# Performance work log

Measured on AMD Instinct MI355X. Metric: run time of the kernel, lower is better.

The kernel has to match this reference:

```python
import jax, jax.numpy as jnp
import numpy as np

N, E, D_IN, H, OUT = 50000, 800000, 128, 256, 2
BN_EPS = 1e-5
LN_EPS = 1e-5


def _xavier(k, fi, fo):
    lim = float(np.sqrt(6.0 / (fi + fo)))
    return jax.random.uniform(k, (fi, fo), minval=-lim, maxval=lim, dtype=jnp.float32)


def setup_inputs() -> dict:
    key = jax.random.key(0)
    ks = jax.random.split(key, 8)
    return {
        "x": jax.random.normal(ks[0], (N, D_IN), dtype=jnp.float32),
        "edge_index": jax.random.randint(ks[1], (2, E), 0, N, dtype=jnp.int32),
        "feature_scale": jnp.ones((D_IN,), jnp.float32),
        "feature_bias": jnp.zeros((D_IN,), jnp.float32),
        "bn0_g": jnp.ones((D_IN,), jnp.float32),
        "bn0_b": jnp.zeros((D_IN,), jnp.float32),
        "W1": _xavier(ks[2], D_IN, H), "b1": jnp.zeros((H,), jnp.float32),
        "bn1_g": jnp.ones((H,), jnp.float32), "bn1_b": jnp.zeros((H,), jnp.float32),
        "ln1_g": jnp.ones((H,), jnp.float32), "ln1_b": jnp.zeros((H,), jnp.float32),
        "W2": _xavier(ks[3], H, H), "b2": jnp.zeros((H,), jnp.float32),
        "bn2_g": jnp.ones((H,), jnp.float32), "bn2_b": jnp.zeros((H,), jnp.float32),
        "ln2_g": jnp.ones((H,), jnp.float32), "ln2_b": jnp.zeros((H,), jnp.float32),
        "Wout": _xavier(ks[4], H, OUT), "bout": jnp.zeros((OUT,), jnp.float32),
    }


def _batchnorm(x, g, b):
    # training-mode BatchNorm1d: batch stats over node axis, biased variance
    mu = jnp.mean(x, axis=0)
    var = jnp.mean(jnp.square(x - mu), axis=0)
    return g * (x - mu) * jax.lax.rsqrt(var + BN_EPS) + b


def _layernorm(x, g, b):
    mu = jnp.mean(x, axis=-1, keepdims=True)
    var = jnp.mean(jnp.square(x - mu), axis=-1, keepdims=True)
    return g * (x - mu) * jax.lax.rsqrt(var + LN_EPS) + b


def _gcn(x, W, b, src, dst, dinv):
    # PyG GCNConv with self-loops: D^{-1/2}(A+I)D^{-1/2} X W + b
    h = x @ W                                   # [N, F]
    norm = (dinv[src] * dinv[dst])[:, None]     # [E, 1]
    msg = h[src] * norm                         # [E, F] (dominant traffic)
    agg = jax.ops.segment_sum(msg, dst, num_segments=N)
    return agg + (dinv * dinv)[:, None] * h + b


def _forward(x, feature_scale, feature_bias, bn0_g, bn0_b,
             W1, b1, bn1_g, bn1_b, ln1_g, ln1_b,
             W2, b2, bn2_g, bn2_b, ln2_g, ln2_b,
             Wout, bout, edge_index):
    src, dst = edge_index[0], edge_index[1]
    deg = jax.ops.segment_sum(jnp.ones((E,), x.dtype), dst, num_segments=N) + 1.0
    dinv = jax.lax.rsqrt(deg)

    h = x * feature_scale + feature_bias
    h = _batchnorm(h, bn0_g, bn0_b)            # input_bn; dropout = identity (eval)

    # layer 0 (no residual: i == 0)
    h1 = _gcn(h, W1, b1, src, dst, dinv)
    h1 = jax.nn.relu(h1)
    h1 = _batchnorm(h1, bn1_g, bn1_b)
    h1 = _layernorm(h1, ln1_g, ln1_b)

    # layer 1 (residual add, shapes match)
    h2 = _gcn(h1, W2, b2, src, dst, dinv)
    h2 = jax.nn.relu(h2)
    h2 = _batchnorm(h2, bn2_g, bn2_b)
    h2 = _layernorm(h2, ln2_g, ln2_b)
    h2 = h2 + h1

    return h2 @ Wout + bout


def reference(x, edge_index, feature_scale, feature_bias, bn0_g, bn0_b,
              W1, b1, bn1_g, bn1_b, ln1_g, ln1_b,
              W2, b2, bn2_g, bn2_b, ln2_g, ln2_b,
              Wout, bout):
    return _forward(x, feature_scale, feature_bias, bn0_g, bn0_b,
                    W1, b1, bn1_g, bn1_b, ln1_g, ln1_b,
                    W2, b2, bn2_g, bn2_b, ln2_g, ln2_b,
                    Wout, bout, edge_index)
```

## Files before the change

kernel.cpp:

```cpp
#include <hip/hip_runtime.h>
#include <hip/hip_bf16.h>
#include <stdint.h>

#define N_NODES 50000
#define N_EDGES 800000
#define D_IN    128
#define H_DIM   256
#define BN_EPS  1e-5f
#define LN_EPS  1e-5f
#define NBLK2 782
#define SLICE_ELEMS ((size_t)N_NODES * 32)
#define EDGE_CHUNK 4096
#define BN0_BLOCKS 1024
#define TR_BLOCKS 256
#define NBKT 196
#define CHUNK 2048
#define RCHUNKS 391

typedef float v4f __attribute__((ext_vector_type(4)));
typedef float v2f __attribute__((ext_vector_type(2)));
typedef short v8s __attribute__((ext_vector_type(8)));
typedef unsigned v4u __attribute__((ext_vector_type(4)));

__device__ __forceinline__ float bflo(unsigned u){ return __uint_as_float(u << 16); }
__device__ __forceinline__ float bfhi(unsigned u){ return __uint_as_float(u & 0xffff0000u); }
__device__ __forceinline__ unsigned short f2bf(float f){
  unsigned u = __float_as_uint(f);
  u += 0x7fffu + ((u >> 16) & 1u);
  return (unsigned short)(u >> 16);
}
__device__ __forceinline__ unsigned pack2(float a, float b){
  return (unsigned)f2bf(a) | ((unsigned)f2bf(b) << 16);
}

__device__ __forceinline__ int block_excl_scan(int v){
  int t = threadIdx.x;
  int lane = t & 63, w = t >> 6;
  int inc = v;
  #pragma unroll
  for (int m = 1; m < 64; m <<= 1){
    int o = __shfl_up(inc, m, 64);
    if (lane >= m) inc += o;
  }
  __shared__ int wsum[4];
  if (lane == 63) wsum[w] = inc;
  __syncthreads();
  int base = 0;
  #pragma unroll
  for (int j = 0; j < 4; ++j) if (j < w) base += wsum[j];
  return base + inc - v;
}

__global__ __launch_bounds__(256) void bn0r1_k(const int* ei, const float* x,
                                               const float* fs, const float* fb,
                                               float* S, float* Q, int* ghist){
  int b = blockIdx.x, t = threadIdx.x;
  if (b >= BN0_BLOCKS){
    __shared__ int lh[NBKT];
    int b2 = b - BN0_BLOCKS;
    for (int i = t; i < NBKT; i += 256) lh[i] = 0;
    __syncthreads();
    int e0 = b2 * CHUNK;
    int n = min(CHUNK, N_EDGES - e0);
    for (int i = t; i < n; i += 256)
      atomicAdd(&lh[ei[N_EDGES + e0 + i] >> 8], 1);
    __syncthreads();
    if (t < NBKT && lh[t] > 0) atomicAdd(&ghist[t], lh[t]);
    return;
  }
  int cl = t & 31, rg = t >> 5;
  int c = cl * 4;
  float4 fs4 = *(const float4*)(fs + c);
  float4 fb4 = *(const float4*)(fb + c);
  float s0=0,s1=0,s2=0,s3=0,q0=0,q1=0,q2=0,q3=0;
  for (int row = b * 8 + rg; row < N_NODES; row += BN0_BLOCKS * 8){
    float4 xv = *(const float4*)(x + (size_t)row * D_IN + c);
    float v0 = xv.x * fs4.x + fb4.x;
    float v1 = xv.y * fs4.y + fb4.y;
    float v2 = xv.z * fs4.z + fb4.z;
    float v3 = xv.w * fs4.w + fb4.w;
    s0 += v0; s1 += v1; s2 += v2; s3 += v3;
    q0 += v0*v0; q1 += v1*v1; q2 += v2*v2; q3 += v3*v3;
  }
  __shared__ float red[256][8];
  red[t][0]=s0; red[t][1]=s1; red[t][2]=s2; red[t][3]=s3;
  red[t][4]=q0; red[t][5]=q1; red[t][6]=q2; red[t][7]=q3;
  __syncthreads();
  float* Sr = S + (b & 7) * D_IN;
  float* Qr = Q + (b & 7) * D_IN;
  if (t < 32){
    float a[8];
    #pragma unroll
    for (int i = 0; i < 8; ++i) a[i] = red[t][i];
    for (int j = 1; j < 8; ++j)
      #pragma unroll
      for (int i = 0; i < 8; ++i) a[i] += red[t + 32*j][i];
    #pragma unroll
    for (int i = 0; i < 4; ++i){ atomicAdd(&Sr[t*4+i], a[i]); atomicAdd(&Qr[t*4+i], a[4+i]); }
  }
}

__global__ __launch_bounds__(256) void r3_k(const int* ei, const int* ghist, int* gcursor, unsigned* ebuf){
  __shared__ unsigned short dstS[CHUNK];
  __shared__ int lh[NBKT], cb[NBKT], sbb[NBKT];
  int t = threadIdx.x;
  int v = (t < NBKT) ? ghist[t] : 0;
  int epre = block_excl_scan(v);
  if (t < NBKT){ sbb[t] = epre; lh[t] = 0; }
  __syncthreads();
  int e0 = blockIdx.x * CHUNK;
  int n = min(CHUNK, N_EDGES - e0);
  for (int i = t; i < n; i += 256){
    int d = ei[N_EDGES + e0 + i];
    dstS[i] = (unsigned short)d;
    atomicAdd(&lh[d >> 8], 1);
  }
  __syncthreads();
  if (t < NBKT && lh[t] > 0) cb[t] = sbb[t] + atomicAdd(&gcursor[t], lh[t]);
  __syncthreads();
  if (t < NBKT) lh[t] = 0;
  __syncthreads();
  for (int i = t; i < n; i += 256){
    int d = dstS[i];
    int bkt = d >> 8;
    int r = atomicAdd(&lh[bkt], 1);
    unsigned src = (unsigned)ei[e0 + i];
    ebuf[cb[bkt] + r] = ((unsigned)(d & 255) << 16) | src;
  }
}

__global__ __launch_bounds__(256) void sortprep_k(const unsigned* ebuf, const int* ghist,
                                                  int* perm, int* offs, float* dinv,
                                                  unsigned short* edges,
                                                  const float* W1, const float* W2,
                                                  unsigned short* W1t, unsigned short* W2t){
  int b = blockIdx.x, t = threadIdx.x;
  if (b < NBKT){
    __shared__ int h[256], dh[128], ep_s[128], W_s[128], lc[128], curs[256], sbb[NBKT + 1];
    int gv = (t < NBKT) ? ghist[t] : 0;
    int gpre = block_excl_scan(gv);
    if (t < NBKT) sbb[t] = gpre;
    if (t == NBKT - 1) sbb[NBKT] = gpre + gv;
    h[t] = 0;
    if (t < 128){ dh[t] = 0; lc[t] = 0; }
    __syncthreads();
    int lo = sbb[b], hi = sbb[b + 1];
    for (int i = lo + t; i < hi; i += 256)
      atomicAdd(&h[(ebuf[i] >> 16) & 255], 1);
    __syncthreads();
    int node = b * 256 + t;
    bool valid = node < N_NODES;
    int deg = valid ? h[t] : 0;
    if (valid) atomicAdd(&dh[min(deg, 127)], 1);
    __syncthreads();
    int cv = (t < 128) ? dh[t] : 0;
    int e1 = block_excl_scan(cv);
    __syncthreads();
    int e2 = block_excl_scan((t < 128) ? cv * t : 0);
    __syncthreads();
    if (t < 128){ ep_s[t] = e1; W_s[t] = e2; }
    __syncthreads();
    if (valid){
      int bin = min(deg, 127);
      int r = atomicAdd(&lc[bin], 1);
      int pl = ep_s[bin] + r;
      int pos = b * 256 + pl;
      int off = lo + W_s[bin] + (pl - ep_s[bin]) * deg;
      perm[pos] = node;
      offs[pos] = off;
      dinv[node] = rsqrtf((float)deg + 1.0f);
      curs[t] = off;
    }
    __syncthreads();
    for (int i = lo + t; i < hi; i += 256){
      unsigned u = ebuf[i];
      int l8 = (u >> 16) & 255;
      int pos = atomicAdd(&curs[l8], 1);
      edges[pos] = (unsigned short)(u & 0xffffu);
    }
    if (b == 0 && t == 0) offs[N_NODES] = N_EDGES;
    return;
  }
  int i = (b - NBKT) * 256 + t;
  if (i < D_IN * H_DIM){
    int r = i / H_DIM, c = i % H_DIM;
    W1t[c * D_IN + r] = f2bf(W1[i]);
  }
  if (i < H_DIM * H_DIM){
    int r = i / H_DIM, c = i % H_DIM;
    W2t[c * H_DIM + r] = f2bf(W2[i]);
  }
}

__global__ __launch_bounds__(512) void gemm1_k(const float* x, const float* S, const float* Q,
                                               const float* fs, const float* fb,
                                               const float* gg, const float* bb,
                                               const unsigned short* Bt, const float* dinv,
                                               unsigned short* C, int M){
  __shared__ __align__(16) short smem[16896];
  __shared__ float ac[128], cc[128], dvs[128];
  short* As = smem;
  short* Bs = smem + 128 * 40;
  int t = threadIdx.x;
  int m0 = blockIdx.x * 128;
  int lane = t & 63, w = t >> 6;
  int wr = w >> 2, wc = w & 3;
  int fr = lane & 15, quad = lane >> 4;
  if (t < 128){
    dvs[t] = (m0 + t < M) ? dinv[m0 + t] : 0.0f;
    float s8 = 0.f, q8 = 0.f;
    #pragma unroll
    for (int rep = 0; rep < 8; ++rep){ s8 += S[rep * D_IN + t]; q8 += Q[rep * D_IN + t]; }
    const float invN = 1.0f / N_NODES;
    float mu = s8 * invN;
    float rs = rsqrtf(q8 * invN - mu * mu + BN_EPS);
    float a = gg[t] * rs * fs[t];
    ac[t] = a;
    cc[t] = gg[t] * rs * (fb[t] - mu) + bb[t];
  }
  __syncthreads();
  v4f acc[4][4] = {};
  int ar = t >> 2, aq = t & 3;
  int br = t >> 1, bh = t & 1;
  for (int k0 = 0; k0 < D_IN; k0 += 32){
    __syncthreads();
    {
      int arow = m0 + ar;
      int c = k0 + aq * 8;
      float4 xv0 = {0,0,0,0}, xv1 = {0,0,0,0};
      if (arow < M){
        xv0 = *(const float4*)(x + (size_t)arow * D_IN + c);
        xv1 = *(const float4*)(x + (size_t)arow * D_IN + c + 4);
      }
      float4 a0 = *(const float4*)(&ac[c]);
      float4 a1 = *(const float4*)(&ac[c + 4]);
      float4 c0 = *(const float4*)(&cc[c]);
      float4 c1 = *(const float4*)(&cc[c + 4]);
      uint4 o;
      o.x = pack2(a0.x * xv0.x + c0.x, a0.y * xv0.y + c0.y);
      o.y = pack2(a0.z * xv0.z + c0.z, a0.w * xv0.w + c0.w);
      o.z = pack2(a1.x * xv1.x + c1.x, a1.y * xv1.y + c1.y);
      o.w = pack2(a1.z * xv1.z + c1.z, a1.w * xv1.w + c1.w);
      *(uint4*)(&As[ar * 40 + aq * 8]) = o;
    }
    {
      const unsigned short* bp = Bt + (size_t)br * D_IN + k0 + bh * 16;
      uint4 b0 = *(const uint4*)(bp);
      uint4 b1 = *(const uint4*)(bp + 8);
      *(uint4*)(&Bs[br * 40 + bh * 16]) = b0;
      *(uint4*)(&Bs[br * 40 + bh * 16 + 8]) = b1;
    }
    __syncthreads();
    v8s af[4], bf[4];
    #pragma unroll
    for (int mi = 0; mi < 4; ++mi)
      af[mi] = *(const v8s*)(&As[(wr * 64 + mi * 16 + fr) * 40 + quad * 8]);
    #pragma unroll
    for (int ni = 0; ni < 4; ++ni)
      bf[ni] = *(const v8s*)(&Bs[(wc * 64 + ni * 16 + fr) * 40 + quad * 8]);
    #pragma unroll
    for (int mi = 0; mi < 4; ++mi)
      #pragma unroll
      for (int ni = 0; ni < 4; ++ni)
        acc[mi][ni] = __builtin_amdgcn_mfma_f32_16x16x32_bf16(af[mi], bf[ni], acc[mi][ni], 0, 0, 0);
  }
  short* Cs = smem;
  #pragma unroll
  for (int h = 0; h < 2; ++h){
    __syncthreads();
    if (wr == h){
      #pragma unroll
      for (int mi = 0; mi < 4; ++mi)
        #pragma unroll
        for (int ni = 0; ni < 4; ++ni)
          #pragma unroll
          for (int r = 0; r < 4; ++r){
            int row = mi * 16 + quad * 4 + r;
            int col = wc * 64 + ni * 16 + fr;
            Cs[row * 264 + col] = (short)f2bf(acc[mi][ni][r] * dvs[h * 64 + row]);
          }
    }
    __syncthreads();
    int orow = t >> 3, o8 = t & 7;
    int grow = m0 + h * 64 + orow;
    if (grow < M){
      const short* src = &Cs[orow * 264 + o8 * 32];
      unsigned short* dst = C + (size_t)o8 * SLICE_ELEMS + (size_t)grow * 32;
      v8s v0 = *(const v8s*)(src);
      v8s v1 = *(const v8s*)(src + 8);
      v8s v2 = *(const v8s*)(src + 16);
      v8s v3 = *(const v8s*)(src + 24);
      *(v8s*)(dst) = v0;
      *(v8s*)(dst + 8) = v1;
      *(v8s*)(dst + 16) = v2;
      *(v8s*)(dst + 24) = v3;
    }
  }
}

__global__ __launch_bounds__(256) void gemm2_k(const unsigned short* gB,
                                               const float* Sg, const float* Qg,
                                               const float* bng, const float* bnb,
                                               const float* lng, const float* lnb,
                                               const unsigned short* Bt, const float* dinv,
                                               unsigned short* C, unsigned short* h1, int M){
  __shared__ __align__(16) short smem[16896];
  __shared__ float scs[256], shs[256], lgs[256], lbs[256], muS[64], rsS[64], dvs[64];
  short* As = smem;
  short* Bs = smem + 64 * 40;
  int t = threadIdx.x;
  int m0 = blockIdx.x * 64;
  int lane = t & 63, w = t >> 6;
  int fr = lane & 15, quad = lane >> 4;
  if (t < 64) dvs[t] = (m0 + t < M) ? dinv[m0 + t] : 0.0f;
  {
    const float invN = 1.0f / N_NODES;
    float mu = Sg[t] * invN;
    float rs = rsqrtf(Qg[t] * invN - mu * mu + BN_EPS);
    float s = bng[t] * rs;
    scs[t] = s; shs[t] = bnb[t] - s * mu;
    lgs[t] = lng[t]; lbs[t] = lnb[t];
  }
  __syncthreads();
  {
    int r = t >> 2, q = t & 3;
    int grow = m0 + r;
    float sum = 0.f, sq = 0.f;
    if (grow < M){
      #pragma unroll
      for (int j = 0; j < 8; ++j){
        int c = q * 64 + j * 8;
        uint4 u = *(const uint4*)(gB + (size_t)grow * H_DIM + c);
        float4 s0 = *(const float4*)(&scs[c]);
        float4 s1 = *(const float4*)(&scs[c + 4]);
        float4 h0 = *(const float4*)(&shs[c]);
        float4 h4 = *(const float4*)(&shs[c + 4]);
        float v0 = s0.x * bflo(u.x) + h0.x;
        float v1 = s0.y * bfhi(u.x) + h0.y;
        float v2 = s0.z * bflo(u.y) + h0.z;
        float v3 = s0.w * bfhi(u.y) + h0.w;
        float v4 = s1.x * bflo(u.z) + h4.x;
        float v5 = s1.y * bfhi(u.z) + h4.y;
        float v6 = s1.z * bflo(u.w) + h4.z;
        float v7 = s1.w * bfhi(u.w) + h4.w;
        sum += v0+v1+v2+v3+v4+v5+v6+v7;
        sq  += v0*v0+v1*v1+v2*v2+v3*v3+v4*v4+v5*v5+v6*v6+v7*v7;
      }
    }
    sum += __shfl_xor(sum, 1, 64); sum += __shfl_xor(sum, 2, 64);
    sq  += __shfl_xor(sq, 1, 64);  sq  += __shfl_xor(sq, 2, 64);
    if (q == 0){
      float mu = sum * (1.0f / H_DIM);
      float var = sq * (1.0f / H_DIM) - mu * mu;
      muS[r] = mu;
      rsS[r] = rsqrtf(var + LN_EPS);
    }
  }
  v4f acc[4][4] = {};
  int sr = t >> 2;
  int sk = (t & 3) << 3;
  for (int k0 = 0; k0 < H_DIM; k0 += 32){
    __syncthreads();
    {
      int arow = m0 + sr;
      uint4 av = {0,0,0,0};
      if (arow < M){
        int c = k0 + sk;
        uint4 u = *(const uint4*)(gB + (size_t)arow * H_DIM + c);
        float mu = muS[sr], rs = rsS[sr];
        float4 s0 = *(const float4*)(&scs[c]);
        float4 s1 = *(const float4*)(&scs[c + 4]);
        float4 h0 = *(const float4*)(&shs[c]);
        float4 h4 = *(const float4*)(&shs[c + 4]);
        float4 g0 = *(const float4*)(&lgs[c]);
        float4 g1 = *(const float4*)(&lgs[c + 4]);
        float4 b0 = *(const float4*)(&lbs[c]);
        float4 b1 = *(const float4*)(&lbs[c + 4]);
        float y0 = g0.x * ((s0.x * bflo(u.x) + h0.x) - mu) * rs + b0.x;
        float y1 = g0.y * ((s0.y * bfhi(u.x) + h0.y) - mu) * rs + b0.y;
        float y2 = g0.z * ((s0.z * bflo(u.y) + h0.z) - mu) * rs + b0.z;
        float y3 = g0.w * ((s0.w * bfhi(u.y) + h0.w) - mu) * rs + b0.w;
        float y4 = g1.x * ((s1.x * bflo(u.z) + h4.x) - mu) * rs + b1.x;
        float y5 = g1.y * ((s1.y * bfhi(u.z) + h4.y) - mu) * rs + b1.y;
        float y6 = g1.z * ((s1.z * bflo(u.w) + h4.z) - mu) * rs + b1.z;
        float y7 = g1.w * ((s1.w * bfhi(u.w) + h4.w) - mu) * rs + b1.w;
        av.x = pack2(y0, y1); av.y = pack2(y2, y3);
        av.z = pack2(y4, y5); av.w = pack2(y6, y7);
        *(uint4*)(h1 + (size_t)arow * H_DIM + c) = av;
      }
      *(uint4*)(&As[sr * 40 + sk]) = av;
    }
    #pragma unroll
    for (int j = 0; j < 4; ++j){
      int brow = sr + 64 * j;
      uint4 bv = *(const uint4*)(Bt + (size_t)brow * H_DIM + k0 + sk);
      *(uint4*)(&Bs[brow * 40 + sk]) = bv;
    }
    __syncthreads();
    v8s af[4], bf[4];
    #pragma unroll
    for (int mi = 0; mi < 4; ++mi)
      af[mi] = *(const v8s*)(&As[(mi * 16 + fr) * 40 + quad * 8]);
    #pragma unroll
    for (int ni = 0; ni < 4; ++ni)
      bf[ni] = *(const v8s*)(&Bs[(w * 64 + ni * 16 + fr) * 40 + quad * 8]);
    #pragma unroll
    for (int mi = 0; mi < 4; ++mi)
      #pragma unroll
      for (int ni = 0; ni < 4; ++ni)
        acc[mi][ni] = __builtin_amdgcn_mfma_f32_16x16x32_bf16(af[mi], bf[ni], acc[mi][ni], 0, 0, 0);
  }
  __syncthreads();
  short* Cs = smem;
  #pragma unroll
  for (int mi = 0; mi < 4; ++mi)
    #pragma unroll
    for (int ni = 0; ni < 4; ++ni)
      #pragma unroll
      for (int r = 0; r < 4; ++r){
        int row = mi * 16 + quad * 4 + r;
        int col = w * 64 + ni * 16 + fr;
        Cs[row * 264 + col] = (short)f2bf(acc[mi][ni][r] * dvs[row]);
      }
  __syncthreads();
  int orow = t >> 2;
  int grow = m0 + orow;
  if (grow < M){
    #pragma unroll
    for (int j = 0; j < 4; ++j){
      int oc = (t & 3) * 16 + 64 * j;
      v8s v0 = *(const v8s*)(&Cs[orow * 264 + oc]);
      v8s v1 = *(const v8s*)(&Cs[orow * 264 + oc + 8]);
      *(v8s*)(&C[(size_t)(oc >> 5) * SLICE_ELEMS + (size_t)grow * 32 + (oc & 31)]) = v0;
      int oc1 = oc + 8;
      *(v8s*)(&C[(size_t)(oc1 >> 5) * SLICE_ELEMS + (size_t)grow * 32 + (oc1 & 31)]) = v1;
    }
  }
}

#define ACCP(u, A) { v2f d_ = {bflo(u), bfhi(u)}; A += d_; }
#define ACC8(vv) ACCP(vv.x, A0) ACCP(vv.y, A1) ACCP(vv.z, A2) ACCP(vv.w, A3)

__global__ __launch_bounds__(256, 4) void agg_k(const unsigned short* hs, const int* offsets,
                                                const unsigned short* edges, const int* perm,
                                                const float* dinv, const float* bias,
                                                unsigned short* g, float* Sg, float* Qg){
  __shared__ unsigned eds32[EDGE_CHUNK / 2];
  __shared__ float wps[4][4][16];
  int t = threadIdx.x;
  int lane = t & 63;
  int wv = t >> 6;
  int slice = blockIdx.x & 7;
  int l4 = lane & 3;
  int grp = blockIdx.x >> 3;
  int nb = grp * 64;
  int idx = nb + (t >> 2);
  int lastn = min(nb + 64, N_NODES);
  int blk0 = offsets[nb];
  int base = blk0 & ~1;
  int blkN = offsets[lastn];
  const unsigned* gsrc = (const unsigned*)(edges + base);
  int nu = min((blkN - base + 1) >> 1, EDGE_CHUNK / 2);
  for (int i = t; i < nu; i += 256)
    eds32[i] = gsrc[i];
  __syncthreads();
  bool act = idx < N_NODES;
  int node = act ? perm[idx] : 0;
  float dvv = act ? dinv[node] : 0.f;
  const uint4* hb4 = (const uint4*)(hs + (size_t)slice * SLICE_ELEMS);
  float4 bb0 = *(const float4*)(bias + slice * 32 + l4 * 8);
  float4 bb1 = *(const float4*)(bias + slice * 32 + l4 * 8 + 4);
  uint4 sv = hb4[(size_t)node * 4 + l4];
  v2f A0 = {bflo(sv.x), bfhi(sv.x)};
  v2f A1 = {bflo(sv.y), bfhi(sv.y)};
  v2f A2 = {bflo(sv.z), bfhi(sv.z)};
  v2f A3 = {bflo(sv.w), bfhi(sv.w)};
  int e  = act ? offsets[idx] : 0;
  int e1 = act ? offsets[idx + 1] : 0;
  if ((e & 1) && e < e1){
    int ru = (e - base) >> 1;
    unsigned d = (ru < EDGE_CHUNK / 2) ? eds32[ru] : gsrc[ru];
    uint4 vv = hb4[(size_t)(d >> 16) * 4 + l4];
    ACC8(vv);
    ++e;
  }
  for (; e + 16 <= e1; e += 16){
    int ru = (e - base) >> 1;
    unsigned dd[8];
    if (ru + 8 <= EDGE_CHUNK / 2){
      #pragma unroll
      for (int j = 0; j < 8; ++j) dd[j] = eds32[ru + j];
    } else {
      #pragma unroll
      for (int j = 0; j < 8; ++j) dd[j] = gsrc[ru + j];
    }
    uint4 v[16];
    #pragma unroll
    for (int j = 0; j < 8; ++j){
      v[2*j]   = hb4[(size_t)(dd[j] & 0xffffu) * 4 + l4];
      v[2*j+1] = hb4[(size_t)(dd[j] >> 16)     * 4 + l4];
    }
    #pragma unroll
    for (int j = 0; j < 16; ++j){ ACC8(v[j]); }
  }
  if (e + 8 <= e1){
    int ru = (e - base) >> 1;
    unsigned dd[4];
    if (ru + 4 <= EDGE_CHUNK / 2){
      #pragma unroll
      for (int j = 0; j < 4; ++j) dd[j] = eds32[ru + j];
    } else {
      #pragma unroll
      for (int j = 0; j < 4; ++j) dd[j] = gsrc[ru + j];
    }
    uint4 v[8];
    #pragma unroll
    for (int j = 0; j < 4; ++j){
      v[2*j]   = hb4[(size_t)(dd[j] & 0xffffu) * 4 + l4];
      v[2*j+1] = hb4[(size_t)(dd[j] >> 16)     * 4 + l4];
    }
    #pragma unroll
    for (int j = 0; j < 8; ++j){ ACC8(v[j]); }
    e += 8;
  }
  if (e + 4 <= e1){
    int ru = (e - base) >> 1;
    unsigned dd0, dd1;
    if (ru + 2 <= EDGE_CHUNK / 2){
      dd0 = eds32[ru]; dd1 = eds32[ru + 1];
    } else {
      dd0 = gsrc[ru]; dd1 = gsrc[ru + 1];
    }
    uint4 v[4];
    v[0] = hb4[(size_t)(dd0 & 0xffffu) * 4 + l4];
    v[1] = hb4[(size_t)(dd0 >> 16)     * 4 + l4];
    v[2] = hb4[(size_t)(dd1 & 0xffffu) * 4 + l4];
    v[3] = hb4[(size_t)(dd1 >> 16)     * 4 + l4];
    #pragma unroll
    for (int j = 0; j < 4; ++j){ ACC8(v[j]); }
    e += 4;
  }
  for (; e < e1; ++e){
    int r = e - base;
    unsigned d = ((r >> 1) < EDGE_CHUNK / 2) ? eds32[r >> 1] : gsrc[r >> 1];
    unsigned s = (r & 1) ? (d >> 16) : (d & 0xffffu);
    uint4 vv = hb4[(size_t)s * 4 + l4];
    ACC8(vv);
  }
  float y0 = act ? fmaxf(dvv * A0.x + bb0.x, 0.f) : 0.f;
  float y1 = act ? fmaxf(dvv * A0.y + bb0.y, 0.f) : 0.f;
  float y2 = act ? fmaxf(dvv * A1.x + bb0.z, 0.f) : 0.f;
  float y3 = act ? fmaxf(dvv * A1.y + bb0.w, 0.f) : 0.f;
  float y4 = act ? fmaxf(dvv * A2.x + bb1.x, 0.f) : 0.f;
  float y5 = act ? fmaxf(dvv * A2.y + bb1.y, 0.f) : 0.f;
  float y6 = act ? fmaxf(dvv * A3.x + bb1.z, 0.f) : 0.f;
  float y7 = act ? fmaxf(dvv * A3.y + bb1.w, 0.f) : 0.f;
  if (act){
    v4u o;
    o.x = pack2(y0, y1); o.y = pack2(y2, y3);
    o.z = pack2(y4, y5); o.w = pack2(y6, y7);
    __builtin_nontemporal_store(o, (v4u*)(g + (size_t)node * H_DIM + slice * 32 + l4 * 8));
  }
  float q0 = y0*y0, q1 = y1*y1, q2 = y2*y2, q3 = y3*y3;
  float q4 = y4*y4, q5 = y5*y5, q6 = y6*y6, q7 = y7*y7;
  #pragma unroll
  for (int m = 4; m < 64; m <<= 1){
    y0 += __shfl_xor(y0, m, 64); y1 += __shfl_xor(y1, m, 64);
    y2 += __shfl_xor(y2, m, 64); y3 += __shfl_xor(y3, m, 64);
    y4 += __shfl_xor(y4, m, 64); y5 += __shfl_xor(y5, m, 64);
    y6 += __shfl_xor(y6, m, 64); y7 += __shfl_xor(y7, m, 64);
    q0 += __shfl_xor(q0, m, 64); q1 += __shfl_xor(q1, m, 64);
    q2 += __shfl_xor(q2, m, 64); q3 += __shfl_xor(q3, m, 64);
    q4 += __shfl_xor(q4, m, 64); q5 += __shfl_xor(q5, m, 64);
    q6 += __shfl_xor(q6, m, 64); q7 += __shfl_xor(q7, m, 64);
  }
  if (lane < 4){
    wps[wv][lane][0] = y0; wps[wv][lane][1] = y1; wps[wv][lane][2] = y2; wps[wv][lane][3] = y3;
    wps[wv][lane][4] = y4; wps[wv][lane][5] = y5; wps[wv][lane][6] = y6; wps[wv][lane][7] = y7;
    wps[wv][lane][8] = q0; wps[wv][lane][9] = q1; wps[wv][lane][10] = q2; wps[wv][lane][11] = q3;
    wps[wv][lane][12] = q4; wps[wv][lane][13] = q5; wps[wv][lane][14] = q6; wps[wv][lane][15] = q7;
  }
  __syncthreads();
  if (t < 64){
    int tl = t >> 4, ti = t & 15;
    float v = wps[0][tl][ti] + wps[1][tl][ti] + wps[2][tl][ti] + wps[3][tl][ti];
    int col32 = tl * 8 + (ti & 7);
    if (ti < 8) atomicAdd(&Sg[slice * 32 + col32], v);
    else        atomicAdd(&Qg[slice * 32 + col32], v);
  }
}

__global__ __launch_bounds__(256) void apply2_k(const unsigned short* g,
                                                const float* Sg, const float* Qg,
                                                const float* bng, const float* bnb,
                                                const float* lng, const float* lnb,
                                                const unsigned short* h1, const float* Wout,
                                                const float* bout, float* out){
  int t = threadIdx.x;
  int lane32 = t & 31;
  int row = blockIdx.x * 8 + (t >> 5);
  if (row >= N_NODES) return;
  int c = lane32 * 8;
  const float invN = 1.0f / N_NODES;
  float4 S0 = *(const float4*)(Sg + c), S1 = *(const float4*)(Sg + c + 4);
  float4 Q0 = *(const float4*)(Qg + c), Q1 = *(const float4*)(Qg + c + 4);
  float4 G0 = *(const float4*)(bng + c), G1 = *(const float4*)(bng + c + 4);
  float4 B0 = *(const float4*)(bnb + c), B1 = *(const float4*)(bnb + c + 4);
  float Sa[8] = {S0.x,S0.y,S0.z,S0.w,S1.x,S1.y,S1.z,S1.w};
  float Qa[8] = {Q0.x,Q0.y,Q0.z,Q0.w,Q1.x,Q1.y,Q1.z,Q1.w};
  float Ga[8] = {G0.x,G0.y,G0.z,G0.w,G1.x,G1.y,G1.z,G1.w};
  float Ba[8] = {B0.x,B0.y,B0.z,B0.w,B1.x,B1.y,B1.z,B1.w};
  float scv[8], shv[8];
  #pragma unroll
  for (int j = 0; j < 8; ++j){
    float mu = Sa[j] * invN;
    float rs = rsqrtf(Qa[j] * invN - mu * mu + BN_EPS);
    float s = Ga[j] * rs;
    scv[j] = s; shv[j] = Ba[j] - s * mu;
  }
  uint4 u = *(const uint4*)(g + (size_t)row * H_DIM + c);
  float v0 = scv[0] * bflo(u.x) + shv[0];
  float v1 = scv[1] * bfhi(u.x) + shv[1];
  float v2 = scv[2] * bflo(u.y) + shv[2];
  float v3 = scv[3] * bfhi(u.y) + shv[3];
  float v4 = scv[4] * bflo(u.z) + shv[4];
  float v5 = scv[5] * bfhi(u.z) + shv[5];
  float v6 = scv[6] * bflo(u.w) + shv[6];
  float v7 = scv[7] * bfhi(u.w) + shv[7];
  float sum = v0+v1+v2+v3+v4+v5+v6+v7;
  float sq  = v0*v0+v1*v1+v2*v2+v3*v3+v4*v4+v5*v5+v6*v6+v7*v7;
  #pragma unroll
  for (int m = 1; m < 32; m <<= 1){ sum += __shfl_xor(sum, m, 64); sq += __shfl_xor(sq, m, 64); }
  float mu = sum * (1.0f / H_DIM);
  float var = sq * (1.0f / H_DIM) - mu * mu;
  float rs = rsqrtf(var + LN_EPS);
  float4 g40 = *(const float4*)(lng + c);
  float4 g41 = *(const float4*)(lng + c + 4);
  float4 b40 = *(const float4*)(lnb + c);
  float4 b41 = *(const float4*)(lnb + c + 4);
  uint4 hr = *(const uint4*)(h1 + (size_t)row * H_DIM + c);
  float y0 = g40.x * (v0 - mu) * rs + b40.x + bflo(hr.x);
  float y1 = g40.y * (v1 - mu) * rs + b40.y + bfhi(hr.x);
  float y2 = g40.z * (v2 - mu) * rs + b40.z + bflo(hr.y);
  float y3 = g40.w * (v3 - mu) * rs + b40.w + bfhi(hr.y);
  float y4 = g41.x * (v4 - mu) * rs + b41.x + bflo(hr.z);
  float y5 = g41.y * (v5 - mu) * rs + b41.y + bfhi(hr.z);
  float y6 = g41.z * (v6 - mu) * rs + b41.z + bflo(hr.w);
  float y7 = g41.w * (v7 - mu) * rs + b41.w + bfhi(hr.w);
  float4 w0 = *(const float4*)(Wout + c * 2);
  float4 w1 = *(const float4*)(Wout + c * 2 + 4);
  float4 w2 = *(const float4*)(Wout + c * 2 + 8);
  float4 w3 = *(const float4*)(Wout + c * 2 + 12);
  float o0 = y0*w0.x + y1*w0.z + y2*w1.x + y3*w1.z + y4*w2.x + y5*w2.z + y6*w3.x + y7*w3.z;
  float o1 = y0*w0.y + y1*w0.w + y2*w1.y + y3*w1.w + y4*w2.y + y5*w2.w + y6*w3.y + y7*w3.w;
  #pragma unroll
  for (int m = 1; m < 32; m <<= 1){ o0 += __shfl_xor(o0, m, 64); o1 += __shfl_xor(o1, m, 64); }
  if (lane32 == 0){
    out[(size_t)row * 2 + 0] = o0 + bout[0];
    out[(size_t)row * 2 + 1] = o1 + bout[1];
  }
}

extern "C" void kernel_launch(void* const* d_in, const int* in_sizes, int n_in,
                              void* d_out, int out_size, void* d_ws, size_t ws_size,
                              hipStream_t stream) {
  const float* x    = (const float*)d_in[0];
  const int*   ei   = (const int*)d_in[1];
  const float* fs   = (const float*)d_in[2];
  const float* fb   = (const float*)d_in[3];
  const float* bn0g = (const float*)d_in[4];
  const float* bn0b = (const float*)d_in[5];
  const float* W1   = (const float*)d_in[6];
  const float* b1   = (const float*)d_in[7];
  const float* bn1g = (const float*)d_in[8];
  const float* bn1b = (const float*)d_in[9];
  const float* ln1g = (const float*)d_in[10];
  const float* ln1b = (const float*)d_in[11];
  const float* W2   = (const float*)d_in[12];
  const float* b2   = (const float*)d_in[13];
  const float* bn2g = (const float*)d_in[14];
  const float* bn2b = (const float*)d_in[15];
  const float* ln2g = (const float*)d_in[16];
  const float* ln2b = (const float*)d_in[17];
  const float* Wout = (const float*)d_in[18];
  const float* bout = (const float*)d_in[19];
  float* out = (float*)d_out;

  char* w = (char*)d_ws;
  float* bn0S  = (float*)(w + 0);
  float* bn0Q  = (float*)(w + 4096);
  int*   ghist  = (int*)(w + 8192);
  int*   gcursor= (int*)(w + 8976);
  float* Sg1   = (float*)(w + 9760);
  float* Qg1   = (float*)(w + 10784);
  float* Sg2   = (float*)(w + 11808);
  float* Qg2   = (float*)(w + 12832);
  const size_t ZERO_BYTES = 13856;
  float* dinv  = (float*)(w + 211584);
  int*   offs  = (int*)(w + 411584);
  int*   perm  = (int*)(w + 611712);
  unsigned short* edges = (unsigned short*)(w + 1011712);
  unsigned short* W1t  = (unsigned short*)(w + 15411712);
  unsigned short* W2t  = (unsigned short*)(w + 15477248);
  unsigned short* hlin = (unsigned short*)(w + 15608320);
  unsigned*       ebuf = (unsigned*)(w + 15608320);
  unsigned short* gbuf = (unsigned short*)(w + 41208320);
  unsigned short* h1   = (unsigned short*)(w + 66808320);

  (void)in_sizes; (void)n_in; (void)out_size; (void)ws_size;

  hipMemsetAsync(d_ws, 0, ZERO_BYTES, stream);

  bn0r1_k<<<BN0_BLOCKS + RCHUNKS, 256, 0, stream>>>(ei, x, fs, fb, bn0S, bn0Q, ghist);
  r3_k<<<RCHUNKS, 256, 0, stream>>>(ei, ghist, gcursor, ebuf);
  sortprep_k<<<NBKT + TR_BLOCKS, 256, 0, stream>>>(
      ebuf, ghist, perm, offs, dinv, edges, W1, W2, W1t, W2t);

  int g1grid = (N_NODES + 127) / 128;
  int g2grid = (N_NODES + 63) / 64;
  int agg_blocks = NBLK2 * 8;

  gemm1_k<<<g1grid, 512, 0, stream>>>(x, bn0S, bn0Q, fs, fb, bn0g, bn0b, W1t, dinv, hlin, N_NODES);
  agg_k<<<agg_blocks, 256, 0, stream>>>(hlin, offs, edges, perm, dinv, b1, gbuf, Sg1, Qg1);

  gemm2_k<<<g2grid, 256, 0, stream>>>(gbuf, Sg1, Qg1, bn1g, bn1b, ln1g, ln1b, W2t, dinv, hlin, h1, N_NODES);
  agg_k<<<agg_blocks, 256, 0, stream>>>(hlin, offs, edges, perm, dinv, b2, gbuf, Sg2, Qg2);
  apply2_k<<<(N_NODES + 7) / 8, 256, 0, stream>>>(gbuf, Sg2, Qg2, bn2g, bn2b, ln2g, ln2b, h1, Wout, bout, out);
}
```

Before: 330.7 us.

## Enlarge gemm2 block tile to 128 rows with 512 threads and 2x4 wave grid

gemm2_k now processes 128 rows per block with 8 waves arranged as 2 row-groups by 4 column-groups, matching gemm1's launch shape. Each W2 tile load into shared memory now serves twice as many output rows, which cuts redundant weight traffic and halves the block count. The epilogue writes the output in two 64-row halves through the existing shared buffer, with each thread storing a contiguous 32-element slice row. This adds extra barriers in the epilogue and gives each block more threads, which may lower occupancy.

```diff
diff --git a/kernel.cpp b/kernel.cpp
--- a/kernel.cpp
+++ b/kernel.cpp
@@ -298,22 +298,23 @@
   }
 }
 
-__global__ __launch_bounds__(256) void gemm2_k(const unsigned short* gB,
+__global__ __launch_bounds__(512) void gemm2_k(const unsigned short* gB,
                                                const float* Sg, const float* Qg,
                                                const float* bng, const float* bnb,
                                                const float* lng, const float* lnb,
                                                const unsigned short* Bt, const float* dinv,
                                                unsigned short* C, unsigned short* h1, int M){
   __shared__ __align__(16) short smem[16896];
-  __shared__ float scs[256], shs[256], lgs[256], lbs[256], muS[64], rsS[64], dvs[64];
+  __shared__ float scs[256], shs[256], lgs[256], lbs[256], muS[128], rsS[128], dvs[128];
   short* As = smem;
-  short* Bs = smem + 64 * 40;
+  short* Bs = smem + 128 * 40;
   int t = threadIdx.x;
-  int m0 = blockIdx.x * 64;
+  int m0 = blockIdx.x * 128;
   int lane = t & 63, w = t >> 6;
+  int wr = w >> 2, wc = w & 3;
   int fr = lane & 15, quad = lane >> 4;
-  if (t < 64) dvs[t] = (m0 + t < M) ? dinv[m0 + t] : 0.0f;
-  {
+  if (t < 128) dvs[t] = (m0 + t < M) ? dinv[m0 + t] : 0.0f;
+  if (t < 256){
     const float invN = 1.0f / N_NODES;
     float mu = Sg[t] * invN;
     float rs = rsqrtf(Qg[t] * invN - mu * mu + BN_EPS);
@@ -357,17 +358,17 @@
     }
   }
   v4f acc[4][4] = {};
-  int sr = t >> 2;
-  int sk = (t & 3) << 3;
+  int ar = t >> 2, aq = t & 3;
+  int br = t >> 1, bh = t & 1;
   for (int k0 = 0; k0 < H_DIM; k0 += 32){
     __syncthreads();
     {
-      int arow = m0 + sr;
+      int arow = m0 + ar;
       uint4 av = {0,0,0,0};
       if (arow < M){
-        int c = k0 + sk;
+        int c = k0 + aq * 8;
         uint4 u = *(const uint4*)(gB + (size_t)arow * H_DIM + c);
-        float mu = muS[sr], rs = rsS[sr];
+        float mu = muS[ar], rs = rsS[ar];
         float4 s0 = *(const float4*)(&scs[c]);
         float4 s1 = *(const float4*)(&scs[c + 4]);
         float4 h0 = *(const float4*)(&shs[c]);
@@ -386,54 +387,61 @@
         float y7 = g1.w * ((s1.w * bfhi(u.w) + h4.w) - mu) * rs + b1.w;
         av.x = pack2(y0, y1); av.y = pack2(y2, y3);
         av.z = pack2(y4, y5); av.w = pack2(y6, y7);
-        *(uint4*)(h1 + (size_t)arow * H_DIM + c) = av;
+        *(uint4*)(h1 + (size_t)arow * H_DIM + (k0 + aq * 8)) = av;
       }
-      *(uint4*)(&As[sr * 40 + sk]) = av;
-    }
-    #pragma unroll
-    for (int j = 0; j < 4; ++j){
-      int brow = sr + 64 * j;
-      uint4 bv = *(const uint4*)(Bt + (size_t)brow * H_DIM + k0 + sk);
-      *(uint4*)(&Bs[brow * 40 + sk]) = bv;
+      *(uint4*)(&As[ar * 40 + aq * 8]) = av;
+    }
+    {
+      const unsigned short* bp = Bt + (size_t)br * H_DIM + k0 + bh * 16;
+      uint4 b0 = *(const uint4*)(bp);
+      uint4 b1 = *(const uint4*)(bp + 8);
+      *(uint4*)(&Bs[br * 40 + bh * 16]) = b0;
+      *(uint4*)(&Bs[br * 40 + bh * 16 + 8]) = b1;
     }
     __syncthreads();
     v8s af[4], bf[4];
     #pragma unroll
     for (int mi = 0; mi < 4; ++mi)
-      af[mi] = *(const v8s*)(&As[(mi * 16 + fr) * 40 + quad * 8]);
+      af[mi] = *(const v8s*)(&As[(wr * 64 + mi * 16 + fr) * 40 + quad * 8]);
     #pragma unroll
     for (int ni = 0; ni < 4; ++ni)
-      bf[ni] = *(const v8s*)(&Bs[(w * 64 + ni * 16 + fr) * 40 + quad * 8]);
+      bf[ni] = *(const v8s*)(&Bs[(wc * 64 + ni * 16 + fr) * 40 + quad * 8]);
     #pragma unroll
     for (int mi = 0; mi < 4; ++mi)
       #pragma unroll
       for (int ni = 0; ni < 4; ++ni)
         acc[mi][ni] = __builtin_amdgcn_mfma_f32_16x16x32_bf16(af[mi], bf[ni], acc[mi][ni], 0, 0, 0);
   }
-  __syncthreads();
   short* Cs = smem;
   #pragma unroll
-  for (int mi = 0; mi < 4; ++mi)
-    #pragma unroll
-    for (int ni = 0; ni < 4; ++ni)
-      #pragma unroll
-      for (int r = 0; r < 4; ++r){
-        int row = mi * 16 + quad * 4 + r;
-        int col = w * 64 + ni * 16 + fr;
-        Cs[row * 264 + col] = (short)f2bf(acc[mi][ni][r] * dvs[row]);
-      }
-  __syncthreads();
-  int orow = t >> 2;
-  int grow = m0 + orow;
-  if (grow < M){
-    #pragma unroll
-    for (int j = 0; j < 4; ++j){
-      int oc = (t & 3) * 16 + 64 * j;
-      v8s v0 = *(const v8s*)(&Cs[orow * 264 + oc]);
-      v8s v1 = *(const v8s*)(&Cs[orow * 264 + oc + 8]);
-      *(v8s*)(&C[(size_t)(oc >> 5) * SLICE_ELEMS + (size_t)grow * 32 + (oc & 31)]) = v0;
-      int oc1 = oc + 8;
-      *(v8s*)(&C[(size_t)(oc1 >> 5) * SLICE_ELEMS + (size_t)grow * 32 + (oc1 & 31)]) = v1;
+  for (int h = 0; h < 2; ++h){
+    __syncthreads();
+    if (wr == h){
+      #pragma unroll
+      for (int mi = 0; mi < 4; ++mi)
+        #pragma unroll
+        for (int ni = 0; ni < 4; ++ni)
+          #pragma unroll
+          for (int r = 0; r < 4; ++r){
+            int row = mi * 16 + quad * 4 + r;
+            int col = wc * 64 + ni * 16 + fr;
+            Cs[row * 264 + col] = (short)f2bf(acc[mi][ni][r] * dvs[h * 64 + row]);
+          }
+    }
+    __syncthreads();
+    int orow = t >> 3, o8 = t & 7;
+    int grow = m0 + h * 64 + orow;
+    if (grow < M){
+      const short* src = &Cs[orow * 264 + o8 * 32];
+      unsigned short* dst = C + (size_t)o8 * SLICE_ELEMS + (size_t)grow * 32;
+      v8s v0 = *(const v8s*)(src);
+      v8s v1 = *(const v8s*)(src + 8);
+      v8s v2 = *(const v8s*)(src + 16);
+      v8s v3 = *(const v8s*)(src + 24);
+      *(v8s*)(dst) = v0;
+      *(v8s*)(dst + 8) = v1;
+      *(v8s*)(dst + 16) = v2;
+      *(v8s*)(dst + 24) = v3;
     }
   }
 }
@@ -717,13 +725,12 @@
       ebuf, ghist, perm, offs, dinv, edges, W1, W2, W1t, W2t);
 
   int g1grid = (N_NODES + 127) / 128;
-  int g2grid = (N_NODES + 63) / 64;
   int agg_blocks = NBLK2 * 8;
 
   gemm1_k<<<g1grid, 512, 0, stream>>>(x, bn0S, bn0Q, fs, fb, bn0g, bn0b, W1t, dinv, hlin, N_NODES);
   agg_k<<<agg_blocks, 256, 0, stream>>>(hlin, offs, edges, perm, dinv, b1, gbuf, Sg1, Qg1);
 
-  gemm2_k<<<g2grid, 256, 0, stream>>>(gbuf, Sg1, Qg1, bn1g, bn1b, ln1g, ln1b, W2t, dinv, hlin, h1, N_NODES);
+  gemm2_k<<<g1grid, 512, 0, stream>>>(gbuf, Sg1, Qg1, bn1g, bn1b, ln1g, ln1b, W2t, dinv, hlin, h1, N_NODES);
   agg_k<<<agg_blocks, 256, 0, stream>>>(hlin, offs, edges, perm, dinv, b2, gbuf, Sg2, Qg2);
   apply2_k<<<(N_NODES + 7) / 8, 256, 0, stream>>>(gbuf, Sg2, Qg2, bn2g, bn2b, ln2g, ln2b, h1, Wout, bout, out);
 }
```

Result: slower. 338.8 us (+2.5%).
